# Kernel tuning notes

Hardware: AMD Instinct MI355X
Metric: run time of the kernel (lower is better)

The kernel has to match this reference:

```python
import jax, jax.numpy as jnp
import numpy as np

N, D, H, C, E, ED, HID = 50000, 160, 5, 32, 800000, 16, 512
EPS = 1e-5  # torch LayerNorm default
NEG_SLOPE = 0.2  # GATv2Conv default negative_slope


def layer_norm(x, g, b):
    mu = x.mean(-1, keepdims=True)
    var = x.var(-1, keepdims=True)  # biased, matches torch LayerNorm
    return (x - mu) * jax.lax.rsqrt(var + EPS) * g + b


def setup_inputs() -> dict:
    key = jax.random.key(0)
    ks = jax.random.split(key, 12)
    p = lambda k, shape: jax.random.normal(k, shape, jnp.float32) * 0.05
    z = lambda *s: jnp.zeros(s, jnp.float32)
    o = lambda *s: jnp.ones(s, jnp.float32)
    return {
        "x": jax.random.normal(ks[0], (N, D), jnp.float32),
        "edge_index": jax.random.randint(ks[1], (2, E), 0, N),
        "edge_attr": jax.random.normal(ks[2], (E, ED), jnp.float32),
        "u": jax.random.normal(ks[3], (1024, 64), jnp.float32),
        "batch": jax.random.randint(ks[4], (N,), 0, 1024),
        # GATv2Conv params (lin_l, lin_r, lin_edge, att, bias)
        "Wl": p(ks[5], (D, H * C)), "bl": z(H * C),
        "Wr": p(ks[6], (D, H * C)), "br": z(H * C),
        "We": p(ks[7], (ED, H * C)),
        "att": p(ks[8], (H, C)),
        "b_gat": z(H * C),
        # norm1
        "g1": o(D), "b1": z(D),
        # output MLP: Linear(D,HID) -> SELU -> LayerNorm(HID) -> Linear(HID,D)
        "W_m1": p(ks[9], (D, HID)), "b_m1": z(HID),
        "g_m": o(HID), "b_m": z(HID),
        "W_m2": p(ks[10], (HID, D)), "b_m2": z(D),
        # norm2
        "g2": o(D), "b2": z(D),
    }


def reference(x, edge_index, edge_attr, u, batch, Wl, bl, Wr, br, We, att, b_gat,
              g1, b1, W_m1, b_m1, g_m, b_m, W_m2, b_m2, g2, b2):
    src, dst = edge_index[0], edge_index[1]  # messages flow src -> dst
    xl = (x @ Wl + bl).reshape(N, H, C)      # source projection
    xr = (x @ Wr + br).reshape(N, H, C)      # target projection
    ea = (edge_attr @ We).reshape(E, H, C)
    # GATv2 scoring: att . leaky_relu(x_l[j] + x_r[i] + e_ij)
    e = jax.nn.leaky_relu(xl[src] + xr[dst] + ea, NEG_SLOPE)   # [E,H,C]
    score = jnp.einsum('ehc,hc->eh', e, att)                   # [E,H]
    # segment softmax over incoming edges of each target node
    mx = jax.ops.segment_max(score, dst, num_segments=N)       # [N,H]
    ex = jnp.exp(score - mx[dst])
    denom = jax.ops.segment_sum(ex, dst, num_segments=N)
    alpha = ex / denom[dst]                                    # [E,H]
    agg = jax.ops.segment_sum(alpha[:, :, None] * xl[src], dst, num_segments=N)
    attn = agg.reshape(N, H * C) + b_gat                       # concat heads
    # residual + norm, MLP, residual + norm (dropout=0)
    out = layer_norm(x + attn, g1, b1)
    h = layer_norm(jax.nn.selu(out @ W_m1 + b_m1), g_m, b_m)
    mlp = h @ W_m2 + b_m2
    return layer_norm(out + mlp, g2, b2)
```

## Files before the change

kernel.cpp:

```cpp
#include <hip/hip_runtime.h>
#include <math.h>

#define N_NODES 50000
#define D 160
#define H 5
#define C 32
#define HC 160
#define E_EDGES 800000
#define ED 16
#define HID 512
#define EPS 1e-5f
#define NEG_SLOPE 0.2f

typedef __attribute__((ext_vector_type(8))) short bf16x8;
typedef __attribute__((ext_vector_type(4))) float f32x4;
typedef __attribute__((ext_vector_type(4))) short short4v;

__device__ inline float bf2f(short s) {
  unsigned u = ((unsigned)(unsigned short)s) << 16;
  return __builtin_bit_cast(float, u);
}
__device__ inline short f2bf(float f) {
  unsigned u = __builtin_bit_cast(unsigned, f);
  u = u + 0x7fffu + ((u >> 16) & 1u);
  return (short)(u >> 16);
}
__device__ inline float selu_f(float v) {
  return 1.0507009873554805f * (v > 0.f ? v : 1.6732632423543772f * (__expf(v) - 1.f));
}

__global__ void prep_weights(const float* __restrict__ Wl, const float* __restrict__ Wr,
                             const float* __restrict__ Wm1, const float* __restrict__ Wm2,
                             const float* __restrict__ We,
                             short* __restrict__ WlT, short* __restrict__ WrT,
                             short* __restrict__ W1T, short* __restrict__ W2T,
                             short* __restrict__ WeTp) {
  int i = blockIdx.x * blockDim.x + threadIdx.x;
  if (i < 25600) { int n = i / 160, k = i % 160; WlT[n*160 + k] = f2bf(Wl[k*160 + n]); return; }
  i -= 25600;
  if (i < 25600) { int n = i / 160, k = i % 160; WrT[n*160 + k] = f2bf(Wr[k*160 + n]); return; }
  i -= 25600;
  if (i < 81920) { int n = i / 160, k = i % 160; W1T[n*160 + k] = f2bf(Wm1[k*512 + n]); return; }
  i -= 81920;
  if (i < 81920) { int n = i / 512, k = i % 512; W2T[n*512 + k] = f2bf(Wm2[k*160 + n]); return; }
  i -= 81920;
  if (i < 5120) { int col = i / 32, k = i % 32;
    WeTp[col*32 + k] = (k < ED) ? f2bf(We[k*160 + col]) : (short)0; }
}

__global__ void convert_x(const float* __restrict__ x, short* __restrict__ xb) {
  int i = blockIdx.x * blockDim.x + threadIdx.x;
  if (i < N_NODES * D / 8) {
    const float4* s = (const float4*)(x + (size_t)i * 8);
    float4 a = s[0], b = s[1];
    bf16x8 o;
    o[0] = f2bf(a.x); o[1] = f2bf(a.y); o[2] = f2bf(a.z); o[3] = f2bf(a.w);
    o[4] = f2bf(b.x); o[5] = f2bf(b.y); o[6] = f2bf(b.z); o[7] = f2bf(b.w);
    *(bf16x8*)(xb + (size_t)i * 8) = o;
  }
}

__global__ __launch_bounds__(256) void proj_mfma(
    const short* __restrict__ xb, const short* __restrict__ WlT, const short* __restrict__ WrT,
    const float* __restrict__ bl, const float* __restrict__ br,
    short* __restrict__ xl, short* __restrict__ xr)
{
  __shared__ short As[64][40];
  int t = threadIdx.x;
  int wave = t >> 6, lane = t & 63;
  int lq = lane >> 4, lc = lane & 15;
  int row0 = blockIdx.x * 64;
  f32x4 accl[10] = {}, accr[10] = {};
  for (int kt = 0; kt < 5; ++kt) {
    int k0 = kt * 32;
    {
      int r = t >> 2, seg = t & 3;
      int gr = min(row0 + r, N_NODES - 1);
      bf16x8 v = *(const bf16x8*)&xb[(size_t)gr * 160 + k0 + seg * 8];
      *(bf16x8*)&As[r][seg * 8] = v;
    }
    __syncthreads();
    bf16x8 af = *(bf16x8*)&As[wave * 16 + lc][lq * 8];
#pragma unroll
    for (int ct = 0; ct < 10; ++ct) {
      int cc = ct * 16 + lc;
      bf16x8 bfl = *(const bf16x8*)&WlT[cc * 160 + k0 + lq * 8];
      accl[ct] = __builtin_amdgcn_mfma_f32_16x16x32_bf16(af, bfl, accl[ct], 0, 0, 0);
      bf16x8 bfr = *(const bf16x8*)&WrT[cc * 160 + k0 + lq * 8];
      accr[ct] = __builtin_amdgcn_mfma_f32_16x16x32_bf16(af, bfr, accr[ct], 0, 0, 0);
    }
    __syncthreads();
  }
#pragma unroll
  for (int ct = 0; ct < 10; ++ct) {
    int col = ct * 16 + lc;
    float bbl = bl[col], bbr = br[col];
#pragma unroll
    for (int rg = 0; rg < 4; ++rg) {
      int row = row0 + wave * 16 + lq * 4 + rg;
      if (row < N_NODES) {
        xl[(size_t)row * 160 + col] = f2bf(accl[ct][rg] + bbl);
        xr[(size_t)row * 160 + col] = f2bf(accr[ct][rg] + bbr);
      }
    }
  }
}

__global__ void count_kernel(const int* __restrict__ ei, int* __restrict__ cnt) {
  int e = blockIdx.x * blockDim.x + threadIdx.x;
  if (e < E_EDGES) atomicAdd(&cnt[ei[E_EDGES + e]], 1);
}

__global__ __launch_bounds__(1024) void scanA(const int* __restrict__ cnt,
                                              int* __restrict__ pinc, int* __restrict__ bsum) {
  int b = blockIdx.x, t = threadIdx.x;
  int i = b * 1024 + t;
  int v = (i < N_NODES) ? cnt[i] : 0;
  int lane = t & 63, wid = t >> 6;
  int s = v;
#pragma unroll
  for (int off = 1; off < 64; off <<= 1) {
    int u = __shfl_up(s, off, 64);
    if (lane >= off) s += u;
  }
  __shared__ int ws[16];
  if (lane == 63) ws[wid] = s;
  __syncthreads();
  if (wid == 0) {
    int w = (lane < 16) ? ws[lane] : 0;
#pragma unroll
    for (int off = 1; off < 16; off <<= 1) {
      int u = __shfl_up(w, off, 64);
      if (lane >= off) w += u;
    }
    if (lane < 16) ws[lane] = w;
  }
  __syncthreads();
  int incl = s + (wid > 0 ? ws[wid - 1] : 0);
  if (i < N_NODES) pinc[i] = incl;
  if (t == 1023) bsum[b] = incl;
}

__global__ void scanB(const int* __restrict__ bsum, int* __restrict__ boff) {
  int t = threadIdx.x;
  int v = (t < 49) ? bsum[t] : 0;
  int s = v;
#pragma unroll
  for (int off = 1; off < 64; off <<= 1) {
    int u = __shfl_up(s, off, 64);
    if (t >= off) s += u;
  }
  if (t < 49) boff[t] = s - v;
}

__global__ __launch_bounds__(1024) void scanC(const int* __restrict__ pinc,
                                              const int* __restrict__ boff,
                                              int* __restrict__ offs) {
  int b = blockIdx.x, t = threadIdx.x;
  int i = b * 1024 + t;
  if (i < N_NODES) offs[i + 1] = pinc[i] + boff[b];
  if (i == 0) offs[0] = 0;
}

__global__ void scatter3(const int* __restrict__ ei, const float* __restrict__ eattr,
                         const int* __restrict__ offs, int* __restrict__ cursor,
                         int* __restrict__ srcm, short* __restrict__ eacsr) {
  int e = blockIdx.x * blockDim.x + threadIdx.x;
  if (e < E_EDGES) {
    int dst = ei[E_EDGES + e];
    int src = ei[e];
    int slot = atomicAdd(&cursor[dst], 1);
    int j = offs[dst] + slot;
    srcm[j] = src * 160;
    const float4* s = (const float4*)&eattr[(size_t)e * ED];
    float4 v0 = s[0], v1 = s[1], v2 = s[2], v3 = s[3];
    short* o = eacsr + (size_t)j * ED;
    short4v w0, w1, w2, w3;
    w0[0]=f2bf(v0.x); w0[1]=f2bf(v0.y); w0[2]=f2bf(v0.z); w0[3]=f2bf(v0.w);
    w1[0]=f2bf(v1.x); w1[1]=f2bf(v1.y); w1[2]=f2bf(v1.z); w1[3]=f2bf(v1.w);
    w2[0]=f2bf(v2.x); w2[1]=f2bf(v2.y); w2[2]=f2bf(v2.z); w2[3]=f2bf(v2.w);
    w3[0]=f2bf(v3.x); w3[1]=f2bf(v3.y); w3[2]=f2bf(v3.z); w3[3]=f2bf(v3.w);
    *(short4v*)(o + 0) = w0; *(short4v*)(o + 4) = w1;
    *(short4v*)(o + 8) = w2; *(short4v*)(o + 12) = w3;
  }
}

__global__ __launch_bounds__(256) void attn_fused(
    const short* __restrict__ eacsr, const int* __restrict__ srcm,
    const short* __restrict__ WeTp, const short* __restrict__ xl, const short* __restrict__ xr,
    const float* __restrict__ att, const float* __restrict__ x,
    const float* __restrict__ b_gat, const float* __restrict__ g1, const float* __restrict__ b1,
    const int* __restrict__ offs,
    float* __restrict__ outb, short* __restrict__ outb_bf)
{
  __shared__ short xt[4][16][168];
  int t = threadIdx.x;
  int wave = t >> 6, lane = t & 63;
  int lq = lane >> 4, lc = lane & 15;
  int i = blockIdx.x * 4 + wave;
  int e0 = offs[i], e1 = offs[i + 1];
  short* myt = &xt[wave][0][0];

  int segE[5], segS[5];
#pragma unroll
  for (int p = 0; p < 5; ++p) {
    int g = p * 64 + lane;
    int e = (g * 3277) >> 16;
    segE[p] = e;
    segS[p] = g - e * 20;
  }

  float aggc[10] = {};
  float den[5] = {};
  const f32x4 zero4 = {};

  for (int j0 = e0; j0 < e1; j0 += 16) {
#pragma unroll
    for (int p = 0; p < 5; ++p) {
      int j = j0 + segE[p];
      if (j > e1 - 1) j = e1 - 1;
      int srow = srcm[j];
      bf16x8 v = *(const bf16x8*)&xl[(size_t)srow + segS[p] * 8];
      *(bf16x8*)&myt[segE[p] * 168 + segS[p] * 8] = v;
    }
    bf16x8 af = {};
    if (lq < 2) {
      int jr = min(j0 + lc, e1 - 1);
      af = *(const bf16x8*)&eacsr[(size_t)jr * ED + lq * 8];
    }
    bool ok[4];
#pragma unroll
    for (int rg = 0; rg < 4; ++rg) ok[rg] = (j0 + lq * 4 + rg) < e1;

    float partial[5][4] = {};
#pragma unroll
    for (int half = 0; half < 2; ++half) {
      f32x4 acc[5];
#pragma unroll
      for (int cs = 0; cs < 5; ++cs) {
        int ct = half * 5 + cs;
        bf16x8 bfv = *(const bf16x8*)&WeTp[(ct * 16 + lc) * 32 + lq * 8];
        acc[cs] = __builtin_amdgcn_mfma_f32_16x16x32_bf16(af, bfv, zero4, 0, 0, 0);
      }
#pragma unroll
      for (int cs = 0; cs < 5; ++cs) {
        int ct = half * 5 + cs;
        int col = ct * 16 + lc;
        float attv = att[col];
        float xrv = bf2f(xr[(size_t)i * 160 + col]);
#pragma unroll
        for (int rg = 0; rg < 4; ++rg) {
          float xlv = bf2f(myt[(lq * 4 + rg) * 168 + col]);
          float z = acc[cs][rg] + xlv + xrv;
          z = fmaxf(z, NEG_SLOPE * z);
          partial[ct >> 1][rg] = fmaf(z, attv, partial[ct >> 1][rg]);
        }
      }
    }
#pragma unroll
    for (int hh = 0; hh < 5; ++hh) {
#pragma unroll
      for (int rg = 0; rg < 4; ++rg) {
        float p = partial[hh][rg];
        p += __shfl_xor(p, 1, 64);
        p += __shfl_xor(p, 2, 64);
        p += __shfl_xor(p, 4, 64);
        p += __shfl_xor(p, 8, 64);
        float ex = ok[rg] ? __expf(p) : 0.f;
        den[hh] += ex;
        partial[hh][rg] = ex;
      }
    }
#pragma unroll
    for (int ct = 0; ct < 10; ++ct) {
      int col = ct * 16 + lc;
#pragma unroll
      for (int rg = 0; rg < 4; ++rg) {
        float xlv = bf2f(myt[(lq * 4 + rg) * 168 + col]);
        aggc[ct] = fmaf(partial[ct >> 1][rg], xlv, aggc[ct]);
      }
    }
  }
#pragma unroll
  for (int ct = 0; ct < 10; ++ct) {
    aggc[ct] += __shfl_xor(aggc[ct], 16, 64);
    aggc[ct] += __shfl_xor(aggc[ct], 32, 64);
  }
#pragma unroll
  for (int hh = 0; hh < 5; ++hh) {
    den[hh] += __shfl_xor(den[hh], 16, 64);
    den[hh] += __shfl_xor(den[hh], 32, 64);
  }
  float val[10];
  float s1 = 0.f, s2 = 0.f;
#pragma unroll
  for (int ct = 0; ct < 10; ++ct) {
    float d = den[ct >> 1];
    float attn = (d > 0.f) ? aggc[ct] / d : 0.f;
    float v = x[(size_t)i * 160 + ct * 16 + lc] + attn + b_gat[ct * 16 + lc];
    val[ct] = v;
    s1 += v; s2 += v * v;
  }
#pragma unroll
  for (int m = 1; m <= 8; m <<= 1) { s1 += __shfl_xor(s1, m, 64); s2 += __shfl_xor(s2, m, 64); }
  float mu = s1 * (1.f / 160.f);
  float var = s2 * (1.f / 160.f) - mu * mu;
  float rstd = rsqrtf(var + EPS);
  if (lq == 0) {
#pragma unroll
    for (int ct = 0; ct < 10; ++ct) {
      int col = ct * 16 + lc;
      float o = (val[ct] - mu) * rstd * g1[col] + b1[col];
      outb[(size_t)i * 160 + col] = o;
      outb_bf[(size_t)i * 160 + col] = f2bf(o);
    }
  }
}

__global__ __launch_bounds__(256) void mlp1_mfma(
    const short* __restrict__ ab, const short* __restrict__ W1T,
    const float* __restrict__ b1m, const float* __restrict__ gm, const float* __restrict__ bm,
    short* __restrict__ h)
{
  __shared__ short As[32][40];
  __shared__ float ps1[4][32], ps2[4][32];
  int t = threadIdx.x;
  int wave = t >> 6, lane = t & 63;
  int lq = lane >> 4, lc = lane & 15;
  int row0 = blockIdx.x * 32;
  f32x4 acc[2][8] = {};
  for (int kt = 0; kt < 5; ++kt) {
    int k0 = kt * 32;
    if (t < 128) {
      int r = t >> 2, seg = t & 3;
      int gr = min(row0 + r, N_NODES - 1);
      bf16x8 v = *(const bf16x8*)&ab[(size_t)gr * 160 + k0 + seg * 8];
      *(bf16x8*)&As[r][seg * 8] = v;
    }
    __syncthreads();
    bf16x8 af0 = *(bf16x8*)&As[lc][lq * 8];
    bf16x8 af1 = *(bf16x8*)&As[16 + lc][lq * 8];
#pragma unroll
    for (int ct = 0; ct < 8; ++ct) {
      int cc = wave * 128 + ct * 16 + lc;
      bf16x8 bfv = *(const bf16x8*)&W1T[cc * 160 + k0 + lq * 8];
      acc[0][ct] = __builtin_amdgcn_mfma_f32_16x16x32_bf16(af0, bfv, acc[0][ct], 0, 0, 0);
      acc[1][ct] = __builtin_amdgcn_mfma_f32_16x16x32_bf16(af1, bfv, acc[1][ct], 0, 0, 0);
    }
    __syncthreads();
  }
  float s1[2][4] = {}, s2[2][4] = {};
#pragma unroll
  for (int rt = 0; rt < 2; ++rt)
#pragma unroll
    for (int ct = 0; ct < 8; ++ct)
#pragma unroll
      for (int rg = 0; rg < 4; ++rg) {
        int cc = wave * 128 + ct * 16 + lc;
        float v = selu_f(acc[rt][ct][rg] + b1m[cc]);
        acc[rt][ct][rg] = v;
        s1[rt][rg] += v; s2[rt][rg] += v * v;
      }
#pragma unroll
  for (int m = 1; m <= 8; m <<= 1) {
#pragma unroll
    for (int rt = 0; rt < 2; ++rt)
#pragma unroll
      for (int rg = 0; rg < 4; ++rg) {
        s1[rt][rg] += __shfl_xor(s1[rt][rg], m, 64);
        s2[rt][rg] += __shfl_xor(s2[rt][rg], m, 64);
      }
  }
  if (lc == 0) {
#pragma unroll
    for (int rt = 0; rt < 2; ++rt)
#pragma unroll
      for (int rg = 0; rg < 4; ++rg) {
        ps1[wave][rt * 16 + lq * 4 + rg] = s1[rt][rg];
        ps2[wave][rt * 16 + lq * 4 + rg] = s2[rt][rg];
      }
  }
  __syncthreads();
  float mu[2][4], rstd[2][4];
#pragma unroll
  for (int rt = 0; rt < 2; ++rt)
#pragma unroll
    for (int rg = 0; rg < 4; ++rg) {
      int rl = rt * 16 + lq * 4 + rg;
      float a = ps1[0][rl] + ps1[1][rl] + ps1[2][rl] + ps1[3][rl];
      float b = ps2[0][rl] + ps2[1][rl] + ps2[2][rl] + ps2[3][rl];
      float m_ = a * (1.f / 512.f);
      float var = b * (1.f / 512.f) - m_ * m_;
      mu[rt][rg] = m_; rstd[rt][rg] = rsqrtf(var + EPS);
    }
#pragma unroll
  for (int rt = 0; rt < 2; ++rt)
#pragma unroll
    for (int ct = 0; ct < 8; ++ct)
#pragma unroll
      for (int rg = 0; rg < 4; ++rg) {
        int row = row0 + rt * 16 + lq * 4 + rg;
        int cc = wave * 128 + ct * 16 + lc;
        if (row < N_NODES)
          h[(size_t)row * 512 + cc] =
              f2bf((acc[rt][ct][rg] - mu[rt][rg]) * rstd[rt][rg] * gm[cc] + bm[cc]);
      }
}

__global__ __launch_bounds__(256) void mlp2_mfma(
    const short* __restrict__ hb, const short* __restrict__ W2T,
    const float* __restrict__ b2m, const float* __restrict__ outb,
    const float* __restrict__ g2, const float* __restrict__ b2,
    float* __restrict__ y)
{
  __shared__ short As[128][72];
  int t = threadIdx.x;
  int wave = t >> 6, lane = t & 63;
  int lq = lane >> 4, lc = lane & 15;
  int row0 = blockIdx.x * 128;
  f32x4 acc[2][10] = {};
  for (int kt = 0; kt < 8; ++kt) {
    int k0 = kt * 64;
    __syncthreads();
#pragma unroll
    for (int q = 0; q < 4; ++q) {
      int idx = t + 256 * q;
      int r = idx >> 3, seg = idx & 7;
      int gr = min(row0 + r, N_NODES - 1);
      *(bf16x8*)&As[r][seg * 8] = *(const bf16x8*)&hb[(size_t)gr * 512 + k0 + seg * 8];
    }
    __syncthreads();
#pragma unroll
    for (int ks = 0; ks < 2; ++ks) {
      bf16x8 af0 = *(bf16x8*)&As[wave * 32 + lc][ks * 32 + lq * 8];
      bf16x8 af1 = *(bf16x8*)&As[wave * 32 + 16 + lc][ks * 32 + lq * 8];
#pragma unroll
      for (int ct = 0; ct < 10; ++ct) {
        bf16x8 bfv = *(const bf16x8*)&W2T[(ct * 16 + lc) * 512 + k0 + ks * 32 + lq * 8];
        acc[0][ct] = __builtin_amdgcn_mfma_f32_16x16x32_bf16(af0, bfv, acc[0][ct], 0, 0, 0);
        acc[1][ct] = __builtin_amdgcn_mfma_f32_16x16x32_bf16(af1, bfv, acc[1][ct], 0, 0, 0);
      }
    }
  }
  float s1[2][4] = {}, s2[2][4] = {};
#pragma unroll
  for (int rt = 0; rt < 2; ++rt)
#pragma unroll
    for (int ct = 0; ct < 10; ++ct) {
      int col = ct * 16 + lc;
#pragma unroll
      for (int rg = 0; rg < 4; ++rg) {
        int rowl = min(row0 + wave * 32 + rt * 16 + lq * 4 + rg, N_NODES - 1);
        float v = acc[rt][ct][rg] + b2m[col] + outb[(size_t)rowl * 160 + col];
        acc[rt][ct][rg] = v;
        s1[rt][rg] += v; s2[rt][rg] += v * v;
      }
    }
#pragma unroll
  for (int m = 1; m <= 8; m <<= 1) {
#pragma unroll
    for (int rt = 0; rt < 2; ++rt)
#pragma unroll
      for (int rg = 0; rg < 4; ++rg) {
        s1[rt][rg] += __shfl_xor(s1[rt][rg], m, 64);
        s2[rt][rg] += __shfl_xor(s2[rt][rg], m, 64);
      }
  }
  float mu[2][4], rstd[2][4];
#pragma unroll
  for (int rt = 0; rt < 2; ++rt)
#pragma unroll
    for (int rg = 0; rg < 4; ++rg) {
      float m_ = s1[rt][rg] * (1.f / 160.f);
      float var = s2[rt][rg] * (1.f / 160.f) - m_ * m_;
      mu[rt][rg] = m_; rstd[rt][rg] = rsqrtf(var + EPS);
    }
#pragma unroll
  for (int rt = 0; rt < 2; ++rt)
#pragma unroll
    for (int ct = 0; ct < 10; ++ct) {
      int col = ct * 16 + lc;
#pragma unroll
      for (int rg = 0; rg < 4; ++rg) {
        int row = row0 + wave * 32 + rt * 16 + lq * 4 + rg;
        if (row < N_NODES)
          y[(size_t)row * 160 + col] = (acc[rt][ct][rg] - mu[rt][rg]) * rstd[rt][rg] * g2[col] + b2[col];
      }
    }
}

extern "C" void kernel_launch(void* const* d_in, const int* in_sizes, int n_in,
                              void* d_out, int out_size, void* d_ws, size_t ws_size,
                              hipStream_t stream) {
  const float* x     = (const float*)d_in[0];
  const int*   ei    = (const int*)d_in[1];
  const float* eattr = (const float*)d_in[2];
  const float* Wl    = (const float*)d_in[5];
  const float* bl    = (const float*)d_in[6];
  const float* Wr    = (const float*)d_in[7];
  const float* br    = (const float*)d_in[8];
  const float* We    = (const float*)d_in[9];
  const float* att   = (const float*)d_in[10];
  const float* bgat  = (const float*)d_in[11];
  const float* g1    = (const float*)d_in[12];
  const float* b1    = (const float*)d_in[13];
  const float* Wm1   = (const float*)d_in[14];
  const float* bm1   = (const float*)d_in[15];
  const float* gm    = (const float*)d_in[16];
  const float* bm    = (const float*)d_in[17];
  const float* Wm2   = (const float*)d_in[18];
  const float* bm2   = (const float*)d_in[19];
  const float* g2    = (const float*)d_in[20];
  const float* b2    = (const float*)d_in[21];
  float* y = (float*)d_out;

  char* p = (char*)d_ws;
  auto alloc = [&](size_t bytes) {
    void* q = p;
    p += (bytes + 255) & ~(size_t)255;
    return q;
  };
  short* xb      = (short*)alloc((size_t)N_NODES * 160 * 2);
  short* xlb     = (short*)alloc((size_t)N_NODES * 160 * 2);
  short* xrb     = (short*)alloc((size_t)N_NODES * 160 * 2);
  float* outb    = (float*)alloc((size_t)N_NODES * 160 * 4);
  short* outb_bf = (short*)alloc((size_t)N_NODES * 160 * 2);
  short* hb      = (short*)alloc((size_t)N_NODES * 512 * 2);
  short* eacsr   = (short*)alloc((size_t)E_EDGES * ED * 2);
  int*   srcm    = (int*)alloc((size_t)E_EDGES * 4);
  short* WlT     = (short*)alloc(160 * 160 * 2);
  short* WrT     = (short*)alloc(160 * 160 * 2);
  short* W1T     = (short*)alloc(512 * 160 * 2);
  short* W2T     = (short*)alloc(160 * 512 * 2);
  short* WeTp    = (short*)alloc(160 * 32 * 2);
  int*   cnt     = (int*)alloc((size_t)N_NODES * 4);
  int*   offs    = (int*)alloc((size_t)(N_NODES + 1) * 4);
  int*   cursor  = (int*)alloc((size_t)N_NODES * 4);
  int*   pinc    = (int*)alloc((size_t)N_NODES * 4);
  int*   bsum    = (int*)alloc(64 * 4);
  int*   boff    = (int*)alloc(64 * 4);

  hipMemsetAsync(cnt, 0, (size_t)N_NODES * 4, stream);
  hipMemsetAsync(cursor, 0, (size_t)N_NODES * 4, stream);

  prep_weights<<<(220160 + 255) / 256, 256, 0, stream>>>(Wl, Wr, Wm1, Wm2, We,
                                                         WlT, WrT, W1T, W2T, WeTp);
  convert_x<<<(N_NODES * 160 / 8 + 255) / 256, 256, 0, stream>>>(x, xb);
  count_kernel<<<(E_EDGES + 255) / 256, 256, 0, stream>>>(ei, cnt);
  scanA<<<49, 1024, 0, stream>>>(cnt, pinc, bsum);
  scanB<<<1, 64, 0, stream>>>(bsum, boff);
  scanC<<<49, 1024, 0, stream>>>(pinc, boff, offs);
  scatter3<<<(E_EDGES + 255) / 256, 256, 0, stream>>>(ei, eattr, offs, cursor, srcm, eacsr);
  proj_mfma<<<(N_NODES + 63) / 64, 256, 0, stream>>>(xb, WlT, WrT, bl, br, xlb, xrb);
  attn_fused<<<N_NODES / 4, 256, 0, stream>>>(eacsr, srcm, WeTp, xlb, xrb, att, x,
                                              bgat, g1, b1, offs, outb, outb_bf);
  mlp1_mfma<<<(N_NODES + 31) / 32, 256, 0, stream>>>(outb_bf, W1T, bm1, gm, bm, hb);
  mlp2_mfma<<<(N_NODES + 127) / 128, 256, 0, stream>>>(hb, W2T, bm2, outb, g2, b2, y);
}
```

Before: 677.2 us.

## Fuse x bf16 conversion into projection and drop LDS staging in MLP GEMMs

Removes the separate convert_x kernel and its bf16 buffer: the projection kernel now loads fp32 x directly into registers and converts it to bf16 MFMA fragments. The three GEMM kernels (projection, mlp1, mlp2) stop staging A tiles through shared memory with __syncthreads and read fragments straight from global memory per wave. mlp1 shrinks to 16 rows per block and mlp2 to 64 rows per block (16 per wave). The aim is to cut a launch, a full read/write of x, and the barrier overhead. The cost is less reuse of weight loads across rows and more global/L2 traffic for the weights.

```diff
diff --git a/kernel.cpp b/kernel.cpp
--- a/kernel.cpp
+++ b/kernel.cpp
@@ -48,48 +48,32 @@
     WeTp[col*32 + k] = (k < ED) ? f2bf(We[k*160 + col]) : (short)0; }
 }
 
-__global__ void convert_x(const float* __restrict__ x, short* __restrict__ xb) {
-  int i = blockIdx.x * blockDim.x + threadIdx.x;
-  if (i < N_NODES * D / 8) {
-    const float4* s = (const float4*)(x + (size_t)i * 8);
-    float4 a = s[0], b = s[1];
-    bf16x8 o;
-    o[0] = f2bf(a.x); o[1] = f2bf(a.y); o[2] = f2bf(a.z); o[3] = f2bf(a.w);
-    o[4] = f2bf(b.x); o[5] = f2bf(b.y); o[6] = f2bf(b.z); o[7] = f2bf(b.w);
-    *(bf16x8*)(xb + (size_t)i * 8) = o;
-  }
-}
-
 __global__ __launch_bounds__(256) void proj_mfma(
-    const short* __restrict__ xb, const short* __restrict__ WlT, const short* __restrict__ WrT,
+    const float* __restrict__ x, const short* __restrict__ WlT, const short* __restrict__ WrT,
     const float* __restrict__ bl, const float* __restrict__ br,
     short* __restrict__ xl, short* __restrict__ xr)
 {
-  __shared__ short As[64][40];
   int t = threadIdx.x;
   int wave = t >> 6, lane = t & 63;
   int lq = lane >> 4, lc = lane & 15;
-  int row0 = blockIdx.x * 64;
+  int row0 = blockIdx.x * 64 + wave * 16;
   f32x4 accl[10] = {}, accr[10] = {};
+#pragma unroll
   for (int kt = 0; kt < 5; ++kt) {
-    int k0 = kt * 32;
-    {
-      int r = t >> 2, seg = t & 3;
-      int gr = min(row0 + r, N_NODES - 1);
-      bf16x8 v = *(const bf16x8*)&xb[(size_t)gr * 160 + k0 + seg * 8];
-      *(bf16x8*)&As[r][seg * 8] = v;
-    }
-    __syncthreads();
-    bf16x8 af = *(bf16x8*)&As[wave * 16 + lc][lq * 8];
+    int gr = min(row0 + lc, N_NODES - 1);
+    const float4* pa = (const float4*)&x[(size_t)gr * 160 + kt * 32 + lq * 8];
+    float4 a0 = pa[0], a1 = pa[1];
+    bf16x8 af;
+    af[0] = f2bf(a0.x); af[1] = f2bf(a0.y); af[2] = f2bf(a0.z); af[3] = f2bf(a0.w);
+    af[4] = f2bf(a1.x); af[5] = f2bf(a1.y); af[6] = f2bf(a1.z); af[7] = f2bf(a1.w);
 #pragma unroll
     for (int ct = 0; ct < 10; ++ct) {
       int cc = ct * 16 + lc;
-      bf16x8 bfl = *(const bf16x8*)&WlT[cc * 160 + k0 + lq * 8];
+      bf16x8 bfl = *(const bf16x8*)&WlT[cc * 160 + kt * 32 + lq * 8];
       accl[ct] = __builtin_amdgcn_mfma_f32_16x16x32_bf16(af, bfl, accl[ct], 0, 0, 0);
-      bf16x8 bfr = *(const bf16x8*)&WrT[cc * 160 + k0 + lq * 8];
+      bf16x8 bfr = *(const bf16x8*)&WrT[cc * 160 + kt * 32 + lq * 8];
       accr[ct] = __builtin_amdgcn_mfma_f32_16x16x32_bf16(af, bfr, accr[ct], 0, 0, 0);
     }
-    __syncthreads();
   }
 #pragma unroll
   for (int ct = 0; ct < 10; ++ct) {
@@ -97,7 +81,7 @@
     float bbl = bl[col], bbr = br[col];
 #pragma unroll
     for (int rg = 0; rg < 4; ++rg) {
-      int row = row0 + wave * 16 + lq * 4 + rg;
+      int row = row0 + lq * 4 + rg;
       if (row < N_NODES) {
         xl[(size_t)row * 160 + col] = f2bf(accl[ct][rg] + bbl);
         xr[(size_t)row * 160 + col] = f2bf(accr[ct][rg] + bbr);
@@ -322,89 +306,70 @@
     const float* __restrict__ b1m, const float* __restrict__ gm, const float* __restrict__ bm,
     short* __restrict__ h)
 {
-  __shared__ short As[32][40];
-  __shared__ float ps1[4][32], ps2[4][32];
+  __shared__ float ps1[4][16], ps2[4][16];
   int t = threadIdx.x;
   int wave = t >> 6, lane = t & 63;
   int lq = lane >> 4, lc = lane & 15;
-  int row0 = blockIdx.x * 32;
-  f32x4 acc[2][8] = {};
+  int row0 = blockIdx.x * 16;
+  f32x4 acc[8] = {};
+#pragma unroll
   for (int kt = 0; kt < 5; ++kt) {
-    int k0 = kt * 32;
-    if (t < 128) {
-      int r = t >> 2, seg = t & 3;
-      int gr = min(row0 + r, N_NODES - 1);
-      bf16x8 v = *(const bf16x8*)&ab[(size_t)gr * 160 + k0 + seg * 8];
-      *(bf16x8*)&As[r][seg * 8] = v;
-    }
-    __syncthreads();
-    bf16x8 af0 = *(bf16x8*)&As[lc][lq * 8];
-    bf16x8 af1 = *(bf16x8*)&As[16 + lc][lq * 8];
+    bf16x8 af = *(const bf16x8*)&ab[(size_t)(row0 + lc) * 160 + kt * 32 + lq * 8];
 #pragma unroll
     for (int ct = 0; ct < 8; ++ct) {
       int cc = wave * 128 + ct * 16 + lc;
-      bf16x8 bfv = *(const bf16x8*)&W1T[cc * 160 + k0 + lq * 8];
-      acc[0][ct] = __builtin_amdgcn_mfma_f32_16x16x32_bf16(af0, bfv, acc[0][ct], 0, 0, 0);
-      acc[1][ct] = __builtin_amdgcn_mfma_f32_16x16x32_bf16(af1, bfv, acc[1][ct], 0, 0, 0);
-    }
-    __syncthreads();
-  }
-  float s1[2][4] = {}, s2[2][4] = {};
-#pragma unroll
-  for (int rt = 0; rt < 2; ++rt)
-#pragma unroll
-    for (int ct = 0; ct < 8; ++ct)
-#pragma unroll
-      for (int rg = 0; rg < 4; ++rg) {
-        int cc = wave * 128 + ct * 16 + lc;
-        float v = selu_f(acc[rt][ct][rg] + b1m[cc]);
-        acc[rt][ct][rg] = v;
-        s1[rt][rg] += v; s2[rt][rg] += v * v;
-      }
+      bf16x8 bfv = *(const bf16x8*)&W1T[cc * 160 + kt * 32 + lq * 8];
+      acc[ct] = __builtin_amdgcn_mfma_f32_16x16x32_bf16(af, bfv, acc[ct], 0, 0, 0);
+    }
+  }
+  float s1[4] = {}, s2[4] = {};
+#pragma unroll
+  for (int ct = 0; ct < 8; ++ct) {
+    int cc = wave * 128 + ct * 16 + lc;
+    float bb = b1m[cc];
+#pragma unroll
+    for (int rg = 0; rg < 4; ++rg) {
+      float v = selu_f(acc[ct][rg] + bb);
+      acc[ct][rg] = v;
+      s1[rg] += v; s2[rg] += v * v;
+    }
+  }
 #pragma unroll
   for (int m = 1; m <= 8; m <<= 1) {
 #pragma unroll
-    for (int rt = 0; rt < 2; ++rt)
-#pragma unroll
-      for (int rg = 0; rg < 4; ++rg) {
-        s1[rt][rg] += __shfl_xor(s1[rt][rg], m, 64);
-        s2[rt][rg] += __shfl_xor(s2[rt][rg], m, 64);
-      }
+    for (int rg = 0; rg < 4; ++rg) {
+      s1[rg] += __shfl_xor(s1[rg], m, 64);
+      s2[rg] += __shfl_xor(s2[rg], m, 64);
+    }
   }
   if (lc == 0) {
 #pragma unroll
-    for (int rt = 0; rt < 2; ++rt)
-#pragma unroll
-      for (int rg = 0; rg < 4; ++rg) {
-        ps1[wave][rt * 16 + lq * 4 + rg] = s1[rt][rg];
-        ps2[wave][rt * 16 + lq * 4 + rg] = s2[rt][rg];
-      }
+    for (int rg = 0; rg < 4; ++rg) {
+      ps1[wave][lq * 4 + rg] = s1[rg];
+      ps2[wave][lq * 4 + rg] = s2[rg];
+    }
   }
   __syncthreads();
-  float mu[2][4], rstd[2][4];
-#pragma unroll
-  for (int rt = 0; rt < 2; ++rt)
-#pragma unroll
-    for (int rg = 0; rg < 4; ++rg) {
-      int rl = rt * 16 + lq * 4 + rg;
-      float a = ps1[0][rl] + ps1[1][rl] + ps1[2][rl] + ps1[3][rl];
-      float b = ps2[0][rl] + ps2[1][rl] + ps2[2][rl] + ps2[3][rl];
-      float m_ = a * (1.f / 512.f);
-      float var = b * (1.f / 512.f) - m_ * m_;
-      mu[rt][rg] = m_; rstd[rt][rg] = rsqrtf(var + EPS);
-    }
-#pragma unroll
-  for (int rt = 0; rt < 2; ++rt)
-#pragma unroll
-    for (int ct = 0; ct < 8; ++ct)
-#pragma unroll
-      for (int rg = 0; rg < 4; ++rg) {
-        int row = row0 + rt * 16 + lq * 4 + rg;
-        int cc = wave * 128 + ct * 16 + lc;
-        if (row < N_NODES)
-          h[(size_t)row * 512 + cc] =
-              f2bf((acc[rt][ct][rg] - mu[rt][rg]) * rstd[rt][rg] * gm[cc] + bm[cc]);
-      }
+  float mu[4], rstd[4];
+#pragma unroll
+  for (int rg = 0; rg < 4; ++rg) {
+    int rl = lq * 4 + rg;
+    float a = ps1[0][rl] + ps1[1][rl] + ps1[2][rl] + ps1[3][rl];
+    float b = ps2[0][rl] + ps2[1][rl] + ps2[2][rl] + ps2[3][rl];
+    float m_ = a * (1.f / 512.f);
+    float var = b * (1.f / 512.f) - m_ * m_;
+    mu[rg] = m_; rstd[rg] = rsqrtf(var + EPS);
+  }
+#pragma unroll
+  for (int ct = 0; ct < 8; ++ct) {
+    int cc = wave * 128 + ct * 16 + lc;
+    float gg = gm[cc], bb = bm[cc];
+#pragma unroll
+    for (int rg = 0; rg < 4; ++rg) {
+      int row = row0 + lq * 4 + rg;
+      h[(size_t)row * 512 + cc] = f2bf((acc[ct][rg] - mu[rg]) * rstd[rg] * gg + bb);
+    }
+  }
 }
 
 __global__ __launch_bounds__(256) void mlp2_mfma(
@@ -413,80 +378,58 @@
     const float* __restrict__ g2, const float* __restrict__ b2,
     float* __restrict__ y)
 {
-  __shared__ short As[128][72];
   int t = threadIdx.x;
   int wave = t >> 6, lane = t & 63;
   int lq = lane >> 4, lc = lane & 15;
-  int row0 = blockIdx.x * 128;
-  f32x4 acc[2][10] = {};
-  for (int kt = 0; kt < 8; ++kt) {
-    int k0 = kt * 64;
-    __syncthreads();
-#pragma unroll
-    for (int q = 0; q < 4; ++q) {
-      int idx = t + 256 * q;
-      int r = idx >> 3, seg = idx & 7;
-      int gr = min(row0 + r, N_NODES - 1);
-      *(bf16x8*)&As[r][seg * 8] = *(const bf16x8*)&hb[(size_t)gr * 512 + k0 + seg * 8];
-    }
-    __syncthreads();
-#pragma unroll
-    for (int ks = 0; ks < 2; ++ks) {
-      bf16x8 af0 = *(bf16x8*)&As[wave * 32 + lc][ks * 32 + lq * 8];
-      bf16x8 af1 = *(bf16x8*)&As[wave * 32 + 16 + lc][ks * 32 + lq * 8];
-#pragma unroll
-      for (int ct = 0; ct < 10; ++ct) {
-        bf16x8 bfv = *(const bf16x8*)&W2T[(ct * 16 + lc) * 512 + k0 + ks * 32 + lq * 8];
-        acc[0][ct] = __builtin_amdgcn_mfma_f32_16x16x32_bf16(af0, bfv, acc[0][ct], 0, 0, 0);
-        acc[1][ct] = __builtin_amdgcn_mfma_f32_16x16x32_bf16(af1, bfv, acc[1][ct], 0, 0, 0);
-      }
-    }
-  }
-  float s1[2][4] = {}, s2[2][4] = {};
-#pragma unroll
-  for (int rt = 0; rt < 2; ++rt)
+  int row0 = blockIdx.x * 64 + wave * 16;
+  f32x4 acc[10] = {};
+#pragma unroll
+  for (int kt = 0; kt < 16; ++kt) {
+    int gr = min(row0 + lc, N_NODES - 1);
+    bf16x8 af = *(const bf16x8*)&hb[(size_t)gr * 512 + kt * 32 + lq * 8];
 #pragma unroll
     for (int ct = 0; ct < 10; ++ct) {
-      int col = ct * 16 + lc;
-#pragma unroll
-      for (int rg = 0; rg < 4; ++rg) {
-        int rowl = min(row0 + wave * 32 + rt * 16 + lq * 4 + rg, N_NODES - 1);
-        float v = acc[rt][ct][rg] + b2m[col] + outb[(size_t)rowl * 160 + col];
-        acc[rt][ct][rg] = v;
-        s1[rt][rg] += v; s2[rt][rg] += v * v;
-      }
-    }
+      bf16x8 bfv = *(const bf16x8*)&W2T[(ct * 16 + lc) * 512 + kt * 32 + lq * 8];
+      acc[ct] = __builtin_amdgcn_mfma_f32_16x16x32_bf16(af, bfv, acc[ct], 0, 0, 0);
+    }
+  }
+  float s1[4] = {}, s2[4] = {};
+#pragma unroll
+  for (int ct = 0; ct < 10; ++ct) {
+    int col = ct * 16 + lc;
+#pragma unroll
+    for (int rg = 0; rg < 4; ++rg) {
+      int rowl = min(row0 + lq * 4 + rg, N_NODES - 1);
+      float v = acc[ct][rg] + b2m[col] + outb[(size_t)rowl * 160 + col];
+      acc[ct][rg] = v;
+      s1[rg] += v; s2[rg] += v * v;
+    }
+  }
 #pragma unroll
   for (int m = 1; m <= 8; m <<= 1) {
 #pragma unroll
-    for (int rt = 0; rt < 2; ++rt)
-#pragma unroll
-      for (int rg = 0; rg < 4; ++rg) {
-        s1[rt][rg] += __shfl_xor(s1[rt][rg], m, 64);
-        s2[rt][rg] += __shfl_xor(s2[rt][rg], m, 64);
-      }
-  }
-  float mu[2][4], rstd[2][4];
-#pragma unroll
-  for (int rt = 0; rt < 2; ++rt)
-#pragma unroll
-    for (int rg = 0; rg < 4; ++rg) {
-      float m_ = s1[rt][rg] * (1.f / 160.f);
-      float var = s2[rt][rg] * (1.f / 160.f) - m_ * m_;
-      mu[rt][rg] = m_; rstd[rt][rg] = rsqrtf(var + EPS);
-    }
-#pragma unroll
-  for (int rt = 0; rt < 2; ++rt)
-#pragma unroll
-    for (int ct = 0; ct < 10; ++ct) {
-      int col = ct * 16 + lc;
-#pragma unroll
-      for (int rg = 0; rg < 4; ++rg) {
-        int row = row0 + wave * 32 + rt * 16 + lq * 4 + rg;
-        if (row < N_NODES)
-          y[(size_t)row * 160 + col] = (acc[rt][ct][rg] - mu[rt][rg]) * rstd[rt][rg] * g2[col] + b2[col];
-      }
-    }
+    for (int rg = 0; rg < 4; ++rg) {
+      s1[rg] += __shfl_xor(s1[rg], m, 64);
+      s2[rg] += __shfl_xor(s2[rg], m, 64);
+    }
+  }
+  float mu[4], rstd[4];
+#pragma unroll
+  for (int rg = 0; rg < 4; ++rg) {
+    float m_ = s1[rg] * (1.f / 160.f);
+    float var = s2[rg] * (1.f / 160.f) - m_ * m_;
+    mu[rg] = m_; rstd[rg] = rsqrtf(var + EPS);
+  }
+#pragma unroll
+  for (int ct = 0; ct < 10; ++ct) {
+    int col = ct * 16 + lc;
+#pragma unroll
+    for (int rg = 0; rg < 4; ++rg) {
+      int row = row0 + lq * 4 + rg;
+      if (row < N_NODES)
+        y[(size_t)row * 160 + col] = (acc[ct][rg] - mu[rg]) * rstd[rg] * g2[col] + b2[col];
+    }
+  }
 }
 
 extern "C" void kernel_launch(void* const* d_in, const int* in_sizes, int n_in,
@@ -520,7 +463,6 @@
     p += (bytes + 255) & ~(size_t)255;
     return q;
   };
-  short* xb      = (short*)alloc((size_t)N_NODES * 160 * 2);
   short* xlb     = (short*)alloc((size_t)N_NODES * 160 * 2);
   short* xrb     = (short*)alloc((size_t)N_NODES * 160 * 2);
   float* outb    = (float*)alloc((size_t)N_NODES * 160 * 4);
@@ -545,15 +487,14 @@
 
   prep_weights<<<(220160 + 255) / 256, 256, 0, stream>>>(Wl, Wr, Wm1, Wm2, We,
                                                          WlT, WrT, W1T, W2T, WeTp);
-  convert_x<<<(N_NODES * 160 / 8 + 255) / 256, 256, 0, stream>>>(x, xb);
   count_kernel<<<(E_EDGES + 255) / 256, 256, 0, stream>>>(ei, cnt);
   scanA<<<49, 1024, 0, stream>>>(cnt, pinc, bsum);
   scanB<<<1, 64, 0, stream>>>(bsum, boff);
   scanC<<<49, 1024, 0, stream>>>(pinc, boff, offs);
   scatter3<<<(E_EDGES + 255) / 256, 256, 0, stream>>>(ei, eattr, offs, cursor, srcm, eacsr);
-  proj_mfma<<<(N_NODES + 63) / 64, 256, 0, stream>>>(xb, WlT, WrT, bl, br, xlb, xrb);
+  proj_mfma<<<(N_NODES + 63) / 64, 256, 0, stream>>>(x, WlT, WrT, bl, br, xlb, xrb);
   attn_fused<<<N_NODES / 4, 256, 0, stream>>>(eacsr, srcm, WeTp, xlb, xrb, att, x,
                                               bgat, g1, b1, offs, outb, outb_bf);
-  mlp1_mfma<<<(N_NODES + 31) / 32, 256, 0, stream>>>(outb_bf, W1T, bm1, gm, bm, hb);
-  mlp2_mfma<<<(N_NODES + 127) / 128, 256, 0, stream>>>(hb, W2T, bm2, outb, g2, b2, y);
-}
+  mlp1_mfma<<<N_NODES / 16, 256, 0, stream>>>(outb_bf, W1T, bm1, gm, bm, hb);
+  mlp2_mfma<<<(N_NODES + 63) / 64, 256, 0, stream>>>(hb, W2T, bm2, outb, g2, b2, y);
+}
```

After: 670.3 us. Within noise of the previous version (-1.0%).
